# Optimization experiments

Hardware: AMD Instinct MI355X
Metric: run time of the kernel (lower is better)

The kernel has to match this reference:

```python
import jax, jax.numpy as jnp
import numpy as np
from jax import lax

B, T, L = 2048, 80, 128


def setup_inputs() -> dict:
    key = jax.random.key(0)
    k1, k2, k3, k4, k5 = jax.random.split(key, 5)
    x = jax.random.normal(k1, (B, T, L), dtype=jnp.float32)  # emissions (model logits)
    y = jax.random.randint(k2, (B, T), 0, L)                 # gold tag sequence
    trans = jax.random.normal(k3, (L, L), dtype=jnp.float32) * 0.1
    start_trans = jax.random.normal(k4, (L,), dtype=jnp.float32) * 0.1
    end_trans = jax.random.normal(k5, (L,), dtype=jnp.float32) * 0.1
    return {"x": x, "trans": trans, "start_trans": start_trans,
            "end_trans": end_trans, "y": y}


def reference(x, trans, start_trans, end_trans, y):
    # Linear-chain CRF log-likelihood (TorchCRF semantics, mask = all ones).
    # x: [B,T,L] emissions, y: [B,T] gold tags. Returns [B] log-likelihoods.
    # --- numerator: score of the gold path ---
    emit = jnp.take_along_axis(x, y[..., None], axis=2).squeeze(-1).sum(axis=1)  # [B]
    tr = trans[y[:, :-1], y[:, 1:]].sum(axis=1)                                  # [B]
    numerator = start_trans[y[:, 0]] + emit + tr + end_trans[y[:, -1]]           # [B]
    # --- denominator: log-partition via forward algorithm (scan over time) ---
    alpha0 = start_trans[None, :] + x[:, 0]  # [B,L]
    xt = jnp.swapaxes(x, 0, 1)[1:]           # [T-1,B,L]

    def step(alpha, h_t):
        # alpha[b,i] + trans[i,j] -> logsumexp over i, then add emission h_t[b,j]
        a = jax.nn.logsumexp(alpha[:, :, None] + trans[None, :, :], axis=1) + h_t
        return a, None

    alpha, _ = lax.scan(step, alpha0, xt)
    log_z = jax.nn.logsumexp(alpha + end_trans[None, :], axis=1)  # [B]
    return numerator - log_z
```

## Files before the change

### kernel.cpp

```cpp
#include <hip/hip_runtime.h>
#include <math.h>


#define CRF_B 2048
#define CRF_T 80
#define CRF_L 128

typedef __attribute__((ext_vector_type(8))) short bf16x8_t;
typedef __attribute__((ext_vector_type(4))) float f32x4_t;

__device__ __forceinline__ int pack_bf16_trunc(float lo, float hi) {
    return (int)((__float_as_uint(lo) >> 16) | (__float_as_uint(hi) & 0xFFFF0000u));
}

__global__ __launch_bounds__(256) void crf_v3_kernel(
    const float* __restrict__ x,
    const float* __restrict__ trans,
    const float* __restrict__ start_trans,
    const float* __restrict__ end_trans,
    const int*   __restrict__ y,
    float* __restrict__ out)
{
    const int tid  = threadIdx.x;
    const int w    = tid >> 6;
    const int lane = tid & 63;
    const int quad = lane >> 4;
    const int n16  = lane & 15;
    const int row0 = blockIdx.x * 16;

    __shared__ __attribute__((aligned(16))) short Vb[2][16][136];
    __shared__ __attribute__((aligned(16))) float maxb[2][16][4];
    __shared__ __attribute__((aligned(16))) float sumb[16][4];
    __shared__ float numb[16];

    {
        const int rr = tid >> 4, tt = tid & 15;
        const int bb = row0 + rr;
        const int* yb = y + bb * CRF_T;
        const float* xbn = x + (size_t)bb * CRF_T * CRF_L;
        float p = 0.f;
        for (int t = tt; t < CRF_T; t += 16) {
            const int yt = yb[t];
            p += xbn[t * CRF_L + yt];
            p += (t + 1 < CRF_T) ? trans[yt * CRF_L + yb[t + 1]] : end_trans[yt];
            if (t == 0) p += start_trans[yt];
        }
        p += __shfl_xor(p, 1); p += __shfl_xor(p, 2);
        p += __shfl_xor(p, 4); p += __shfl_xor(p, 8);
        if (tt == 0) numb[rr] = p;
    }

    bf16x8_t Af[2][4];
    #pragma unroll
    for (int mt = 0; mt < 2; ++mt) {
        const int m = 32 * w + 16 * mt + n16;
        #pragma unroll
        for (int kk = 0; kk < 4; ++kk) {
            union { bf16x8_t v; short s[8]; } u;
            #pragma unroll
            for (int j = 0; j < 8; ++j) {
                const int k = 32 * kk + 8 * quad + j;
                const float e = __expf(trans[k * CRF_L + m]);
                u.s[j] = (short)(__float_as_uint(e) >> 16);
            }
            Af[mt][kk] = u.v;
        }
    }

    const int sc0 = 32 * w + 4 * quad;
    const int sc1 = sc0 + 16;
    const float* xr = x + (size_t)(row0 + n16) * CRF_T * CRF_L;

    f32x4_t ex_end[2], st4[2];
    {
        const f32x4_t e0 = *(const f32x4_t*)&end_trans[sc0];
        const f32x4_t e1 = *(const f32x4_t*)&end_trans[sc1];
        #pragma unroll
        for (int r = 0; r < 4; ++r) {
            ex_end[0][r] = __expf(e0[r]);
            ex_end[1][r] = __expf(e1[r]);
        }
        st4[0] = *(const f32x4_t*)&start_trans[sc0];
        st4[1] = *(const f32x4_t*)&start_trans[sc1];
    }

    f32x4_t P[2];
    float invM = 1.f, crun = 0.f;
    f32x4_t xc[2], xn[2];
    xc[0] = *(const f32x4_t*)&xr[sc0];
    xc[1] = *(const f32x4_t*)&xr[sc1];

    for (int t = 0; t < CRF_T; ++t) {
        if (t + 1 < CRF_T) {
            xn[0] = *(const f32x4_t*)&xr[(t + 1) * CRF_L + sc0];
            xn[1] = *(const f32x4_t*)&xr[(t + 1) * CRF_L + sc1];
        }

        if (t == 0) {
            #pragma unroll
            for (int r = 0; r < 4; ++r) {
                P[0][r] = __expf(st4[0][r] + xc[0][r]);
                P[1][r] = __expf(st4[1][r] + xc[1][r]);
            }
        } else {
            const short* vrow = &Vb[(t - 1) & 1][n16][0];
            bf16x8_t Bf[4];
            #pragma unroll
            for (int kk = 0; kk < 4; ++kk)
                Bf[kk] = *(const bf16x8_t*)&vrow[32 * kk + 8 * quad];
            #pragma unroll
            for (int mt = 0; mt < 2; ++mt) {
                f32x4_t acc = {0.f, 0.f, 0.f, 0.f};
                #pragma unroll
                for (int kk = 0; kk < 4; ++kk)
                    acc = __builtin_amdgcn_mfma_f32_16x16x32_bf16(Af[mt][kk], Bf[kk], acc, 0, 0, 0);
                #pragma unroll
                for (int r = 0; r < 4; ++r)
                    P[mt][r] = acc[r] * __expf(xc[mt][r]) * invM;
            }
        }

        if (t < CRF_T - 1) {
            float g = fmaxf(fmaxf(fmaxf(P[0][0], P[0][1]), fmaxf(P[0][2], P[0][3])),
                            fmaxf(fmaxf(P[1][0], P[1][1]), fmaxf(P[1][2], P[1][3])));
            g = fmaxf(g, __shfl_xor(g, 16));
            g = fmaxf(g, __shfl_xor(g, 32));
            if (lane < 16) maxb[t & 1][n16][w] = g;

            short* dst = &Vb[t & 1][n16][0];
            const int d00 = pack_bf16_trunc(P[0][0], P[0][1]);
            const int d01 = pack_bf16_trunc(P[0][2], P[0][3]);
            const int d10 = pack_bf16_trunc(P[1][0], P[1][1]);
            const int d11 = pack_bf16_trunc(P[1][2], P[1][3]);
            *(int2*)&dst[sc0] = make_int2(d00, d01);
            *(int2*)&dst[sc1] = make_int2(d10, d11);

            __syncthreads();

            const f32x4_t mb = *(const f32x4_t*)&maxb[t & 1][n16][0];
            const float M = fmaxf(fmaxf(mb[0], mb[1]), fmaxf(mb[2], mb[3]));
            crun += __logf(M);
            invM = __builtin_amdgcn_rcpf(M);
        }

        xc[0] = xn[0];
        xc[1] = xn[1];
    }

    float sv = 0.f;
    #pragma unroll
    for (int mt = 0; mt < 2; ++mt)
    #pragma unroll
    for (int r = 0; r < 4; ++r)
        sv += P[mt][r] * ex_end[mt][r];
    sv += __shfl_xor(sv, 16);
    sv += __shfl_xor(sv, 32);
    if (lane < 16) sumb[n16][w] = sv;
    __syncthreads();
    if (tid < 16) {
        const f32x4_t sb = *(const f32x4_t*)&sumb[tid][0];
        const float S = sb[0] + sb[1] + sb[2] + sb[3];
        out[row0 + tid] = numb[tid] - (crun + __logf(S));
    }
}

extern "C" void kernel_launch(void* const* d_in, const int* in_sizes, int n_in,
                              void* d_out, int out_size, void* d_ws, size_t ws_size,
                              hipStream_t stream) {
    const float* x     = (const float*)d_in[0];
    const float* trans = (const float*)d_in[1];
    const float* st    = (const float*)d_in[2];
    const float* et    = (const float*)d_in[3];
    const int*   y     = (const int*)d_in[4];
    float* out = (float*)d_out;

    crf_v3_kernel<<<CRF_B / 16, 256, 0, stream>>>(x, trans, st, et, y, out);
}
```

Baseline: 167.3 us.

## Spread batch rows across more blocks and rescale alpha every four steps

Each block now handles 4 real batch rows instead of 16. The 16 MFMA columns hold duplicated copies of those rows, and the grid is four times larger. The intent is to occupy more of the GPU's compute units and spread the x loads more widely, at the cost of redundant MFMA and exp work. The max-based renormalisation, with its shuffles, log and reciprocal, now runs only every fourth time step instead of every step. This shortens the serial per-step chain but lets values grow unscaled for up to four steps, which risks bf16/fp32 overflow or precision loss.

```diff
diff --git a/kernel.cpp b/kernel.cpp
--- a/kernel.cpp
+++ b/kernel.cpp
@@ -5,6 +5,7 @@
 #define CRF_B 2048
 #define CRF_T 80
 #define CRF_L 128
+#define R_REAL 4
 
 typedef __attribute__((ext_vector_type(8))) short bf16x8_t;
 typedef __attribute__((ext_vector_type(4))) float f32x4_t;
@@ -12,8 +13,11 @@
 __device__ __forceinline__ int pack_bf16_trunc(float lo, float hi) {
     return (int)((__float_as_uint(lo) >> 16) | (__float_as_uint(hi) & 0xFFFF0000u));
 }
+__device__ __forceinline__ unsigned short bft(float f) {
+    return (unsigned short)(__float_as_uint(f) >> 16);
+}
 
-__global__ __launch_bounds__(256) void crf_v3_kernel(
+__global__ __launch_bounds__(256) void crf_v6_kernel(
     const float* __restrict__ x,
     const float* __restrict__ trans,
     const float* __restrict__ start_trans,
@@ -26,28 +30,28 @@
     const int lane = tid & 63;
     const int quad = lane >> 4;
     const int n16  = lane & 15;
-    const int row0 = blockIdx.x * 16;
+    const int row0 = blockIdx.x * R_REAL;
+    const int brow = row0 + (n16 & (R_REAL - 1));
 
     __shared__ __attribute__((aligned(16))) short Vb[2][16][136];
-    __shared__ __attribute__((aligned(16))) float maxb[2][16][4];
+    __shared__ __attribute__((aligned(16))) float maxb[16][4];
     __shared__ __attribute__((aligned(16))) float sumb[16][4];
-    __shared__ float numb[16];
+    __shared__ float numb[R_REAL];
 
     {
-        const int rr = tid >> 4, tt = tid & 15;
-        const int bb = row0 + rr;
+        const int bb = row0 + w;
         const int* yb = y + bb * CRF_T;
         const float* xbn = x + (size_t)bb * CRF_T * CRF_L;
         float p = 0.f;
-        for (int t = tt; t < CRF_T; t += 16) {
+        for (int t = lane; t < CRF_T; t += 64) {
             const int yt = yb[t];
             p += xbn[t * CRF_L + yt];
             p += (t + 1 < CRF_T) ? trans[yt * CRF_L + yb[t + 1]] : end_trans[yt];
             if (t == 0) p += start_trans[yt];
         }
-        p += __shfl_xor(p, 1); p += __shfl_xor(p, 2);
-        p += __shfl_xor(p, 4); p += __shfl_xor(p, 8);
-        if (tt == 0) numb[rr] = p;
+        #pragma unroll
+        for (int off = 1; off <= 32; off <<= 1) p += __shfl_xor(p, off);
+        if (lane == 0) numb[w] = p;
     }
 
     bf16x8_t Af[2][4];
@@ -56,12 +60,11 @@
         const int m = 32 * w + 16 * mt + n16;
         #pragma unroll
         for (int kk = 0; kk < 4; ++kk) {
-            union { bf16x8_t v; short s[8]; } u;
+            union { bf16x8_t v; unsigned short s[8]; } u;
             #pragma unroll
             for (int j = 0; j < 8; ++j) {
                 const int k = 32 * kk + 8 * quad + j;
-                const float e = __expf(trans[k * CRF_L + m]);
-                u.s[j] = (short)(__float_as_uint(e) >> 16);
+                u.s[j] = bft(__expf(trans[k * CRF_L + m]));
             }
             Af[mt][kk] = u.v;
         }
@@ -69,7 +72,7 @@
 
     const int sc0 = 32 * w + 4 * quad;
     const int sc1 = sc0 + 16;
-    const float* xr = x + (size_t)(row0 + n16) * CRF_T * CRF_L;
+    const float* xr = x + (size_t)brow * CRF_T * CRF_L;
 
     f32x4_t ex_end[2], st4[2];
     {
@@ -96,6 +99,14 @@
             xn[1] = *(const f32x4_t*)&xr[(t + 1) * CRF_L + sc1];
         }
 
+        const bool ap = (t > 0) && ((t & 3) == 0);
+        if (ap) {
+            const f32x4_t mb = *(const f32x4_t*)&maxb[n16][0];
+            const float M = fmaxf(fmaxf(mb[0], mb[1]), fmaxf(mb[2], mb[3]));
+            crun += __logf(M);
+            invM  = __builtin_amdgcn_rcpf(M);
+        }
+
         if (t == 0) {
             #pragma unroll
             for (int r = 0; r < 4; ++r) {
@@ -115,18 +126,23 @@
                 for (int kk = 0; kk < 4; ++kk)
                     acc = __builtin_amdgcn_mfma_f32_16x16x32_bf16(Af[mt][kk], Bf[kk], acc, 0, 0, 0);
                 #pragma unroll
-                for (int r = 0; r < 4; ++r)
-                    P[mt][r] = acc[r] * __expf(xc[mt][r]) * invM;
+                for (int r = 0; r < 4; ++r) {
+                    float e = __expf(xc[mt][r]);
+                    if (ap) e *= invM;
+                    P[mt][r] = acc[r] * e;
+                }
             }
         }
 
-        if (t < CRF_T - 1) {
+        if (((t & 3) == 3) && (t < CRF_T - 1)) {
             float g = fmaxf(fmaxf(fmaxf(P[0][0], P[0][1]), fmaxf(P[0][2], P[0][3])),
                             fmaxf(fmaxf(P[1][0], P[1][1]), fmaxf(P[1][2], P[1][3])));
             g = fmaxf(g, __shfl_xor(g, 16));
             g = fmaxf(g, __shfl_xor(g, 32));
-            if (lane < 16) maxb[t & 1][n16][w] = g;
+            if (lane < 16) maxb[n16][w] = g;
+        }
 
+        if (t < CRF_T - 1) {
             short* dst = &Vb[t & 1][n16][0];
             const int d00 = pack_bf16_trunc(P[0][0], P[0][1]);
             const int d01 = pack_bf16_trunc(P[0][2], P[0][3]);
@@ -134,13 +150,7 @@
             const int d11 = pack_bf16_trunc(P[1][2], P[1][3]);
             *(int2*)&dst[sc0] = make_int2(d00, d01);
             *(int2*)&dst[sc1] = make_int2(d10, d11);
-
             __syncthreads();
-
-            const f32x4_t mb = *(const f32x4_t*)&maxb[t & 1][n16][0];
-            const float M = fmaxf(fmaxf(mb[0], mb[1]), fmaxf(mb[2], mb[3]));
-            crun += __logf(M);
-            invM = __builtin_amdgcn_rcpf(M);
         }
 
         xc[0] = xn[0];
@@ -157,7 +167,7 @@
     sv += __shfl_xor(sv, 32);
     if (lane < 16) sumb[n16][w] = sv;
     __syncthreads();
-    if (tid < 16) {
+    if (tid < R_REAL) {
         const f32x4_t sb = *(const f32x4_t*)&sumb[tid][0];
         const float S = sb[0] + sb[1] + sb[2] + sb[3];
         out[row0 + tid] = numb[tid] - (crun + __logf(S));
@@ -174,5 +184,5 @@
     const int*   y     = (const int*)d_in[4];
     float* out = (float*)d_out;
 
-    crf_v3_kernel<<<CRF_B / 16, 256, 0, stream>>>(x, trans, st, et, y, out);
+    crf_v6_kernel<<<CRF_B / R_REAL, 256, 0, stream>>>(x, trans, st, et, y, out);
 }
```

Result: no change. 164.3 us (-1.8%).
